# Kernel tuning notes

Hardware: AMD Instinct MI355X
Metric: run time of the kernel (lower is better)

## Reference

```python
import jax, jax.numpy as jnp
import numpy as np

DEPTH = 8
IN_FEATURES = 512
OUT_FEATURES = 256
LEAF_COUNT = 2 ** DEPTH          # 256
GATE_COUNT = LEAF_COUNT - 1      # 255
BATCH = 65536


def setup_inputs() -> dict:
    key = jax.random.key(0)
    k1, k2, k3 = jax.random.split(key, 3)
    x = jax.random.normal(k1, (BATCH, IN_FEATURES), dtype=jnp.float32)
    # gw stored transposed as (in_features, gate_count), kaiming-like scale
    gw = jax.random.normal(k2, (IN_FEATURES, GATE_COUNT), dtype=jnp.float32) * (1.0 / np.sqrt(IN_FEATURES))
    gb = jnp.zeros((GATE_COUNT,), dtype=jnp.float32)
    z = jax.random.normal(k3, (OUT_FEATURES, LEAF_COUNT), dtype=jnp.float32)
    return {"x": x, "gw": gw, "gb": gb, "z": z}


def _leaf_probs(x, gw, gb):
    # gatings: (B, gate_count); node it's left child (2p+1) uses g, right child (2p+2) uses 1-g
    g = jax.nn.sigmoid(x @ gw + gb)
    B = x.shape[0]
    dens = jnp.ones((B, 1), dtype=x.dtype)
    for d in range(DEPTH):  # level-wise vectorized traversal, O(depth) steps
        lo, hi = 2 ** d - 1, 2 ** (d + 1) - 1
        gl = g[:, lo:hi]  # (B, 2^d) gatings at this level
        # interleave [parent*g, parent*(1-g)] -> children order matches heap layout
        dens = jnp.stack([dens * gl, dens * (1.0 - gl)], axis=-1).reshape(B, -1)
    return dens  # (B, leaf_count)


def reference(x, gw, gb, z):
    leaf = _leaf_probs(x, gw, gb)        # (B, L)
    # constant projection: z @ leaf_probs^T, then transpose -> (B, out)
    return leaf @ z.T
```

## Files before the change

kernel.cpp:

```cpp
#include <hip/hip_runtime.h>
#include <stdint.h>


typedef short bf16x8 __attribute__((ext_vector_type(8)));
typedef float f32x4  __attribute__((ext_vector_type(4)));

__device__ __forceinline__ unsigned short f2bf(float f) {
    union { float f; uint32_t u; } c; c.f = f;
    uint32_t u = c.u;
    return (unsigned short)((u + 0x7FFFu + ((u >> 16) & 1u)) >> 16);
}

__global__ void softtree_prep(const float* __restrict__ gw, const float* __restrict__ z,
                              unsigned short* __restrict__ gwt, unsigned short* __restrict__ zb) {
    int tid = blockIdx.x * 256 + threadIdx.x;
    int n = tid >> 9;
    int k = tid & 511;
    float v = (n < 255) ? gw[k * 255 + n] : 0.0f;
    gwt[tid] = f2bf(v);
    if (tid < 65536) zb[tid] = f2bf(z[tid]);
}

__global__ __launch_bounds__(512) void softtree_main(
    const float* __restrict__ x, const float* __restrict__ gb,
    const unsigned short* __restrict__ gwt, const unsigned short* __restrict__ zb,
    float* __restrict__ out)
{
    __shared__ union {
        struct {
            unsigned short xs[64 * 72];
            unsigned short gws[256 * 72];
        } p1;
        float gs[64 * 257];
    } sm;

    const int tid  = threadIdx.x;
    const int lane = tid & 63;
    const int wave = tid >> 6;
    const int q    = lane >> 4;
    const int l15  = lane & 15;
    const int wr   = wave & 3;
    const int wc   = wave >> 2;
    const int R0   = blockIdx.x * 64;

    f32x4 acc[8];
    #pragma unroll
    for (int i = 0; i < 8; ++i) acc[i] = (f32x4){0.f, 0.f, 0.f, 0.f};

    for (int kc = 0; kc < 8; ++kc) {
        const int k0 = kc * 64;
        __syncthreads();
        #pragma unroll
        for (int i = 0; i < 2; ++i) {
            int e   = tid + i * 512;
            int row = e >> 4;
            int kq  = e & 15;
            const float4 v = *(const float4*)(x + (size_t)(R0 + row) * 512 + k0 + kq * 4);
            uint32_t pa = f2bf(v.x) | ((uint32_t)f2bf(v.y) << 16);
            uint32_t pb = f2bf(v.z) | ((uint32_t)f2bf(v.w) << 16);
            *(uint2*)(sm.p1.xs + row * 72 + kq * 4) = make_uint2(pa, pb);
        }
        #pragma unroll
        for (int i = 0; i < 4; ++i) {
            int e  = tid + i * 512;
            int n  = e >> 3;
            int kk = e & 7;
            const uint4 v = *(const uint4*)(gwt + (size_t)n * 512 + k0 + kk * 8);
            *(uint4*)(sm.p1.gws + n * 72 + kk * 8) = v;
        }
        __syncthreads();
        #pragma unroll
        for (int s = 0; s < 2; ++s) {
            bf16x8 afrag = *(const bf16x8*)(sm.p1.xs + (16 * wr + l15) * 72 + s * 32 + q * 8);
            #pragma unroll
            for (int nt = 0; nt < 8; ++nt) {
                bf16x8 bfrag = *(const bf16x8*)(sm.p1.gws + (128 * wc + nt * 16 + l15) * 72 + s * 32 + q * 8);
                acc[nt] = __builtin_amdgcn_mfma_f32_16x16x32_bf16(afrag, bfrag, acc[nt], 0, 0, 0);
            }
        }
    }
    __syncthreads();

    #pragma unroll
    for (int nt = 0; nt < 8; ++nt) {
        int col = 128 * wc + nt * 16 + l15;
        float gbv = (col < 255) ? gb[col] : 0.0f;
        #pragma unroll
        for (int r = 0; r < 4; ++r) {
            int rowl = 16 * wr + 4 * q + r;
            float t = acc[nt][r] + gbv;
            sm.gs[rowl * 257 + col] = 1.0f / (1.0f + __expf(-t));
        }
    }
    __syncthreads();

    const float* gr = sm.gs + (16 * wr + l15) * 257;
    bf16x8 a2[8];
    #pragma unroll
    for (int c = 0; c < 8; ++c) {
        int G = c * 4 + q;
        float p = 1.0f;
        #pragma unroll
        for (int d = 0; d < 5; ++d) {
            int node = (1 << d) - 1 + (G >> (5 - d));
            int bit  = (G >> (4 - d)) & 1;
            float gv = gr[node];
            p *= bit ? (1.0f - gv) : gv;
        }
        float g5 = gr[31 + G];
        float a0 = p * g5, a1 = p - a0;
        float g6a = gr[63 + 2 * G], g6b = gr[64 + 2 * G];
        float b00 = a0 * g6a, b01 = a0 - b00;
        float b10 = a1 * g6b, b11 = a1 - b10;
        float g70 = gr[127 + 4 * G], g71 = gr[128 + 4 * G];
        float g72 = gr[129 + 4 * G], g73 = gr[130 + 4 * G];
        float lf0 = b00 * g70, lf1 = b00 - lf0;
        float lf2 = b01 * g71, lf3 = b01 - lf2;
        float lf4 = b10 * g72, lf5 = b10 - lf4;
        float lf6 = b11 * g73, lf7 = b11 - lf6;
        union { bf16x8 v; uint32_t u[4]; } pk;
        pk.u[0] = f2bf(lf0) | ((uint32_t)f2bf(lf1) << 16);
        pk.u[1] = f2bf(lf2) | ((uint32_t)f2bf(lf3) << 16);
        pk.u[2] = f2bf(lf4) | ((uint32_t)f2bf(lf5) << 16);
        pk.u[3] = f2bf(lf6) | ((uint32_t)f2bf(lf7) << 16);
        a2[c] = pk.v;
    }

    f32x4 acc2[8];
    #pragma unroll
    for (int i = 0; i < 8; ++i) acc2[i] = (f32x4){0.f, 0.f, 0.f, 0.f};
    #pragma unroll
    for (int nt = 0; nt < 8; ++nt) {
        const unsigned short* zrow = zb + (size_t)(128 * wc + nt * 16 + l15) * 256 + q * 8;
        #pragma unroll
        for (int c = 0; c < 8; ++c) {
            bf16x8 bfrag = *(const bf16x8*)(zrow + c * 32);
            acc2[nt] = __builtin_amdgcn_mfma_f32_16x16x32_bf16(a2[c], bfrag, acc2[nt], 0, 0, 0);
        }
    }

    #pragma unroll
    for (int nt = 0; nt < 8; ++nt) {
        int col = 128 * wc + nt * 16 + l15;
        #pragma unroll
        for (int r = 0; r < 4; ++r) {
            int row = R0 + 16 * wr + 4 * q + r;
            out[(size_t)row * 256 + col] = acc2[nt][r];
        }
    }
}

extern "C" void kernel_launch(void* const* d_in, const int* in_sizes, int n_in,
                              void* d_out, int out_size, void* d_ws, size_t ws_size,
                              hipStream_t stream) {
    const float* x  = (const float*)d_in[0];
    const float* gw = (const float*)d_in[1];
    const float* gb = (const float*)d_in[2];
    const float* z  = (const float*)d_in[3];
    float* outp = (float*)d_out;

    unsigned short* gwt = (unsigned short*)d_ws;
    unsigned short* zbf = gwt + 256 * 512;

    softtree_prep<<<512, 256, 0, stream>>>(gw, z, gwt, zbf);
    softtree_main<<<1024, 512, 0, stream>>>(x, gb, gwt, zbf, outp);
}
```

Before: 296.9 us.

## Double-buffer gate GEMM with async LDS loads, 128-row tiles, swizzled LDS, tiled prep

```diff
diff --git a/kernel.cpp b/kernel.cpp
--- a/kernel.cpp
+++ b/kernel.cpp
@@ -1,4 +1,5 @@
 #include <hip/hip_runtime.h>
+#include <hip/hip_bf16.h>
 #include <stdint.h>
 
 
@@ -11,141 +12,220 @@
     return (unsigned short)((u + 0x7FFFu + ((u >> 16) & 1u)) >> 16);
 }
 
-__global__ void softtree_prep(const float* __restrict__ gw, const float* __restrict__ z,
-                              unsigned short* __restrict__ gwt, unsigned short* __restrict__ zb) {
-    int tid = blockIdx.x * 256 + threadIdx.x;
-    int n = tid >> 9;
-    int k = tid & 511;
-    float v = (n < 255) ? gw[k * 255 + n] : 0.0f;
-    gwt[tid] = f2bf(v);
-    if (tid < 65536) zb[tid] = f2bf(z[tid]);
-}
-
-__global__ __launch_bounds__(512) void softtree_main(
+__device__ __forceinline__ uint32_t pkbf(float a, float b) {
+    union { __hip_bfloat162 h; uint32_t u; } cv;
+    cv.h = __float22bfloat162_rn(make_float2(a, b));
+    return cv.u;
+}
+
+__global__ __launch_bounds__(256) void softtree_prep(
+    const float* __restrict__ gw, const float* __restrict__ z,
+    unsigned short* __restrict__ gwt, unsigned short* __restrict__ zb)
+{
+    if (blockIdx.x < 32) {
+        __shared__ float tsm[64][65];
+        const int k0 = (blockIdx.x >> 2) * 64;
+        const int n0 = (blockIdx.x & 3) * 64;
+        const int r = threadIdx.x >> 6;
+        const int c = threadIdx.x & 63;
+        const int n = n0 + c;
+        #pragma unroll
+        for (int i = 0; i < 16; ++i) {
+            int kk = r + i * 4;
+            tsm[kk][c] = (n < 255) ? gw[(size_t)(k0 + kk) * 255 + n] : 0.0f;
+        }
+        __syncthreads();
+        #pragma unroll
+        for (int i = 0; i < 16; ++i) {
+            int nn = r + i * 4;
+            gwt[(size_t)(n0 + nn) * 512 + k0 + c] = f2bf(tsm[c][nn]);
+        }
+    } else {
+        int base = (blockIdx.x - 32) * 1024 + threadIdx.x * 4;
+        const float4 v = *(const float4*)(z + base);
+        ushort4 o;
+        o.x = f2bf(v.x); o.y = f2bf(v.y); o.z = f2bf(v.z); o.w = f2bf(v.w);
+        *(ushort4*)(zb + base) = o;
+    }
+}
+
+__global__ __launch_bounds__(512, 4) void softtree_main(
     const float* __restrict__ x, const float* __restrict__ gb,
     const unsigned short* __restrict__ gwt, const unsigned short* __restrict__ zb,
     float* __restrict__ out)
 {
-    __shared__ union {
-        struct {
-            unsigned short xs[64 * 72];
-            unsigned short gws[256 * 72];
-        } p1;
-        float gs[64 * 257];
-    } sm;
+    __shared__ char smraw[81920];
+    float* gs = (float*)smraw;
 
     const int tid  = threadIdx.x;
     const int lane = tid & 63;
-    const int wave = tid >> 6;
+    const int wv   = tid >> 6;
     const int q    = lane >> 4;
     const int l15  = lane & 15;
-    const int wr   = wave & 3;
-    const int wc   = wave >> 2;
-    const int R0   = blockIdx.x * 64;
-
-    f32x4 acc[8];
-    #pragma unroll
-    for (int i = 0; i < 8; ++i) acc[i] = (f32x4){0.f, 0.f, 0.f, 0.f};
+    const int wr   = wv & 3;
+    const int wc   = wv >> 2;
+    const int R0   = blockIdx.x * 128;
+
+    const int xrow = tid >> 3;
+    const int xkg  = (tid & 7) ^ (xrow & 7);
+    const float* xp0 = x + (size_t)(R0 + xrow) * 512 + xkg * 8;
+    const float* xp1 = xp0 + (size_t)64 * 512;
+    char* xsw0 = smraw + 65536 + tid * 16;
+    char* xsw1 = xsw0 + 8192;
+
+    const int ggate_b = wv * 32 + (lane >> 3);
+    const int gkg     = (lane & 7) ^ ((lane >> 3) & 7);
+    const unsigned short* gwp[4];
+    #pragma unroll
+    for (int j = 0; j < 4; ++j)
+        gwp[j] = gwt + (size_t)(ggate_b + j * 8) * 512 + gkg * 8;
+    const uint32_t gwLds = (uint32_t)(wv * 4) * 1024;
+
+    f32x4 acc[2][8];
+    #pragma unroll
+    for (int t = 0; t < 2; ++t)
+        #pragma unroll
+        for (int i = 0; i < 8; ++i) acc[t][i] = (f32x4){0.f, 0.f, 0.f, 0.f};
+
+    float4 xa0 = *(const float4*)(xp0);
+    float4 xb0 = *(const float4*)(xp0 + 4);
+    float4 xa1 = *(const float4*)(xp1);
+    float4 xb1 = *(const float4*)(xp1 + 4);
+    #pragma unroll
+    for (int j = 0; j < 4; ++j)
+        __builtin_amdgcn_global_load_lds(
+            (const __attribute__((address_space(1))) void*)(gwp[j]),
+            (__attribute__((address_space(3))) void*)(smraw + gwLds + j * 1024),
+            16, 0, 0);
 
     for (int kc = 0; kc < 8; ++kc) {
-        const int k0 = kc * 64;
-        __syncthreads();
-        #pragma unroll
-        for (int i = 0; i < 2; ++i) {
-            int e   = tid + i * 512;
-            int row = e >> 4;
-            int kq  = e & 15;
-            const float4 v = *(const float4*)(x + (size_t)(R0 + row) * 512 + k0 + kq * 4);
-            uint32_t pa = f2bf(v.x) | ((uint32_t)f2bf(v.y) << 16);
-            uint32_t pb = f2bf(v.z) | ((uint32_t)f2bf(v.w) << 16);
-            *(uint2*)(sm.p1.xs + row * 72 + kq * 4) = make_uint2(pa, pb);
-        }
-        #pragma unroll
-        for (int i = 0; i < 4; ++i) {
-            int e  = tid + i * 512;
-            int n  = e >> 3;
-            int kk = e & 7;
-            const uint4 v = *(const uint4*)(gwt + (size_t)n * 512 + k0 + kk * 8);
-            *(uint4*)(sm.p1.gws + n * 72 + kk * 8) = v;
-        }
-        __syncthreads();
+        const int buf = kc & 1;
+        __syncthreads();
+
+        union { uint4 u4; uint32_t u[4]; } w0, w1;
+        w0.u[0] = pkbf(xa0.x, xa0.y); w0.u[1] = pkbf(xa0.z, xa0.w);
+        w0.u[2] = pkbf(xb0.x, xb0.y); w0.u[3] = pkbf(xb0.z, xb0.w);
+        w1.u[0] = pkbf(xa1.x, xa1.y); w1.u[1] = pkbf(xa1.z, xa1.w);
+        w1.u[2] = pkbf(xb1.x, xb1.y); w1.u[3] = pkbf(xb1.z, xb1.w);
+        *(uint4*)xsw0 = w0.u4;
+        *(uint4*)xsw1 = w1.u4;
+
+        __syncthreads();
+
+        if (kc < 7) {
+            const int ko = (kc + 1) * 64;
+            #pragma unroll
+            for (int j = 0; j < 4; ++j)
+                __builtin_amdgcn_global_load_lds(
+                    (const __attribute__((address_space(1))) void*)(gwp[j] + ko),
+                    (__attribute__((address_space(3))) void*)(smraw + (buf ^ 1) * 32768 + gwLds + j * 1024),
+                    16, 0, 0);
+            xa0 = *(const float4*)(xp0 + ko);
+            xb0 = *(const float4*)(xp0 + ko + 4);
+            xa1 = *(const float4*)(xp1 + ko);
+            xb1 = *(const float4*)(xp1 + ko + 4);
+        }
+
         #pragma unroll
         for (int s = 0; s < 2; ++s) {
-            bf16x8 afrag = *(const bf16x8*)(sm.p1.xs + (16 * wr + l15) * 72 + s * 32 + q * 8);
+            const int jx = (4 * s + q) ^ (l15 & 7);
+            bf16x8 a0 = *(const bf16x8*)(smraw + 65536 + ((16 * wr + l15) * 8 + jx) * 16);
+            bf16x8 a1 = *(const bf16x8*)(smraw + 65536 + 8192 + ((16 * wr + l15) * 8 + jx) * 16);
             #pragma unroll
             for (int nt = 0; nt < 8; ++nt) {
-                bf16x8 bfrag = *(const bf16x8*)(sm.p1.gws + (128 * wc + nt * 16 + l15) * 72 + s * 32 + q * 8);
-                acc[nt] = __builtin_amdgcn_mfma_f32_16x16x32_bf16(afrag, bfrag, acc[nt], 0, 0, 0);
-            }
-        }
-    }
-    __syncthreads();
-
+                const int gate = 128 * wc + nt * 16 + l15;
+                bf16x8 b = *(const bf16x8*)(smraw + buf * 32768 + (gate * 8 + jx) * 16);
+                acc[0][nt] = __builtin_amdgcn_mfma_f32_16x16x32_bf16(a0, b, acc[0][nt], 0, 0, 0);
+                acc[1][nt] = __builtin_amdgcn_mfma_f32_16x16x32_bf16(a1, b, acc[1][nt], 0, 0, 0);
+            }
+        }
+    }
+
+    float gbv[8];
     #pragma unroll
     for (int nt = 0; nt < 8; ++nt) {
         int col = 128 * wc + nt * 16 + l15;
-        float gbv = (col < 255) ? gb[col] : 0.0f;
-        #pragma unroll
-        for (int r = 0; r < 4; ++r) {
-            int rowl = 16 * wr + 4 * q + r;
-            float t = acc[nt][r] + gbv;
-            sm.gs[rowl * 257 + col] = 1.0f / (1.0f + __expf(-t));
-        }
-    }
-    __syncthreads();
-
-    const float* gr = sm.gs + (16 * wr + l15) * 257;
-    bf16x8 a2[8];
-    #pragma unroll
-    for (int c = 0; c < 8; ++c) {
-        int G = c * 4 + q;
-        float p = 1.0f;
-        #pragma unroll
-        for (int d = 0; d < 5; ++d) {
-            int node = (1 << d) - 1 + (G >> (5 - d));
-            int bit  = (G >> (4 - d)) & 1;
-            float gv = gr[node];
-            p *= bit ? (1.0f - gv) : gv;
-        }
-        float g5 = gr[31 + G];
-        float a0 = p * g5, a1 = p - a0;
-        float g6a = gr[63 + 2 * G], g6b = gr[64 + 2 * G];
-        float b00 = a0 * g6a, b01 = a0 - b00;
-        float b10 = a1 * g6b, b11 = a1 - b10;
-        float g70 = gr[127 + 4 * G], g71 = gr[128 + 4 * G];
-        float g72 = gr[129 + 4 * G], g73 = gr[130 + 4 * G];
-        float lf0 = b00 * g70, lf1 = b00 - lf0;
-        float lf2 = b01 * g71, lf3 = b01 - lf2;
-        float lf4 = b10 * g72, lf5 = b10 - lf4;
-        float lf6 = b11 * g73, lf7 = b11 - lf6;
-        union { bf16x8 v; uint32_t u[4]; } pk;
-        pk.u[0] = f2bf(lf0) | ((uint32_t)f2bf(lf1) << 16);
-        pk.u[1] = f2bf(lf2) | ((uint32_t)f2bf(lf3) << 16);
-        pk.u[2] = f2bf(lf4) | ((uint32_t)f2bf(lf5) << 16);
-        pk.u[3] = f2bf(lf6) | ((uint32_t)f2bf(lf7) << 16);
-        a2[c] = pk.v;
-    }
-
-    f32x4 acc2[8];
-    #pragma unroll
-    for (int i = 0; i < 8; ++i) acc2[i] = (f32x4){0.f, 0.f, 0.f, 0.f};
-    #pragma unroll
-    for (int nt = 0; nt < 8; ++nt) {
-        const unsigned short* zrow = zb + (size_t)(128 * wc + nt * 16 + l15) * 256 + q * 8;
+        gbv[nt] = (col < 255) ? gb[col] : 0.0f;
+    }
+
+    for (int t = 0; t < 2; ++t) {
+        __syncthreads();
+
+        #pragma unroll
+        for (int nt = 0; nt < 8; ++nt) {
+            const int col = 128 * wc + nt * 16 + l15;
+            #pragma unroll
+            for (int r = 0; r < 4; ++r) {
+                const int rowl = 16 * wr + 4 * q + r;
+                float v = acc[t][nt][r] + gbv[nt];
+                gs[rowl * 258 + col] = 1.0f / (1.0f + __expf(-v));
+            }
+        }
+        __syncthreads();
+
+        const float* gr = gs + (16 * wr + l15) * 258;
+        float g0v = gr[0];
+        float t1v[2] = { g0v, 1.0f - g0v };
+        float t2v[4], t3v[8];
+        #pragma unroll
+        for (int u = 0; u < 2; ++u) {
+            float gl = gr[1 + u];
+            t2v[2 * u] = t1v[u] * gl; t2v[2 * u + 1] = t1v[u] - t2v[2 * u];
+        }
+        #pragma unroll
+        for (int u = 0; u < 4; ++u) {
+            float gl = gr[3 + u];
+            t3v[2 * u] = t2v[u] * gl; t3v[2 * u + 1] = t2v[u] - t3v[2 * u];
+        }
+        bf16x8 a2[8];
         #pragma unroll
         for (int c = 0; c < 8; ++c) {
-            bf16x8 bfrag = *(const bf16x8*)(zrow + c * 32);
-            acc2[nt] = __builtin_amdgcn_mfma_f32_16x16x32_bf16(a2[c], bfrag, acc2[nt], 0, 0, 0);
-        }
-    }
-
-    #pragma unroll
-    for (int nt = 0; nt < 8; ++nt) {
-        int col = 128 * wc + nt * 16 + l15;
-        #pragma unroll
-        for (int r = 0; r < 4; ++r) {
-            int row = R0 + 16 * wr + 4 * q + r;
-            out[(size_t)row * 256 + col] = acc2[nt][r];
+            const int G = c * 4 + q;
+            float p = t3v[c];
+            float g3 = gr[7 + c];
+            p = (q & 2) ? (p - p * g3) : (p * g3);
+            float g4 = gr[15 + 2 * c + (q >> 1)];
+            p = (q & 1) ? (p - p * g4) : (p * g4);
+            float g5 = gr[31 + G];
+            float a0 = p * g5, a1 = p - a0;
+            float g6a = gr[63 + 2 * G], g6b = gr[64 + 2 * G];
+            float b00 = a0 * g6a, b01 = a0 - b00;
+            float b10 = a1 * g6b, b11 = a1 - b10;
+            float g70 = gr[127 + 4 * G], g71 = gr[128 + 4 * G];
+            float g72 = gr[129 + 4 * G], g73 = gr[130 + 4 * G];
+            float lf0 = b00 * g70, lf1 = b00 - lf0;
+            float lf2 = b01 * g71, lf3 = b01 - lf2;
+            float lf4 = b10 * g72, lf5 = b10 - lf4;
+            float lf6 = b11 * g73, lf7 = b11 - lf6;
+            union { bf16x8 v; uint32_t u[4]; } pk;
+            pk.u[0] = pkbf(lf0, lf1);
+            pk.u[1] = pkbf(lf2, lf3);
+            pk.u[2] = pkbf(lf4, lf5);
+            pk.u[3] = pkbf(lf6, lf7);
+            a2[c] = pk.v;
+        }
+
+        f32x4 acc2[8];
+        #pragma unroll
+        for (int i = 0; i < 8; ++i) acc2[i] = (f32x4){0.f, 0.f, 0.f, 0.f};
+        #pragma unroll
+        for (int nt = 0; nt < 8; ++nt) {
+            const unsigned short* zrow = zb + (size_t)(128 * wc + nt * 16 + l15) * 256 + q * 8;
+            #pragma unroll
+            for (int c = 0; c < 8; ++c) {
+                bf16x8 b = *(const bf16x8*)(zrow + c * 32);
+                acc2[nt] = __builtin_amdgcn_mfma_f32_16x16x32_bf16(a2[c], b, acc2[nt], 0, 0, 0);
+            }
+        }
+
+        #pragma unroll
+        for (int nt = 0; nt < 8; ++nt) {
+            const int col = 128 * wc + nt * 16 + l15;
+            #pragma unroll
+            for (int r = 0; r < 4; ++r) {
+                const int row = R0 + t * 64 + 16 * wr + 4 * q + r;
+                out[(size_t)row * 256 + col] = acc2[nt][r];
+            }
         }
     }
 }
@@ -162,6 +242,6 @@
     unsigned short* gwt = (unsigned short*)d_ws;
     unsigned short* zbf = gwt + 256 * 512;
 
-    softtree_prep<<<512, 256, 0, stream>>>(gw, z, gwt, zbf);
-    softtree_main<<<1024, 512, 0, stream>>>(x, gb, gwt, zbf, outp);
-}
+    softtree_prep<<<96, 256, 0, stream>>>(gw, z, gwt, zbf);
+    softtree_main<<<512, 512, 0, stream>>>(x, gb, gwt, zbf, outp);
+}
```

After: 281.6 us. -5.2%, faster.
